# Performance work log

Hardware: AMD Instinct MI355X
Metric: run time of the kernel (lower is better)

Reference implementation:

```python
import jax, jax.numpy as jnp
import numpy as np
from jax import lax

NF, CF, LAT = 128, 3, 512          # n_filter, sobel c_factor (id+gx+gy), lat_size
NL, NC = 3, 4                      # n_layers (img 64 -> 3), n_calls
B, IMG, CH = 16, 64, 3
FIN, FH, FOUT = NF * CF, NF, 2 * NF  # dyna/res block in, hidden, out (gated -> 2*NF)
SPLIT = [NF, NF, NF, 1]
NOUT = sum(SPLIT)                  # 385
CS = NF + NF * 16 + NF * 16 + 16 * 16  # 4480 multi-cut state size
SEG = [FIN * FH, FH, FH * FH, FH, FH * FOUT, FOUT, FIN * FOUT, FOUT]
OFF = np.concatenate([[0], np.cumsum(SEG)]).astype(int)
K = int(OFF[-1])                   # hypernet output size (197376)

SOBEL_X = jnp.array([[-1., 0., 1.], [-2., 0., 2.], [-1., 0., 1.]], jnp.float32) / 8.0
SOBEL_Y = SOBEL_X.T
_g = np.exp(-0.5 * (np.arange(3) - 1.0) ** 2); _g /= _g.sum()
GAUSS = jnp.asarray(np.outer(_g, _g), jnp.float32)  # 3x3 gaussian, sigma=1


def dwconv(x, k2d):
    # depthwise conv, same 3x3 kernel for every channel, padding 1
    C = x.shape[1]
    k = jnp.broadcast_to(k2d.astype(x.dtype), (C, 1, 3, 3))
    return lax.conv_general_dilated(x, k, (1, 1), ((1, 1), (1, 1)),
                                    dimension_numbers=('NCHW', 'OIHW', 'NCHW'),
                                    feature_group_count=C)


def instnorm(x, eps=1e-5):
    m = x.mean((2, 3), keepdims=True)
    v = x.var((2, 3), keepdims=True)
    return (x - m) * lax.rsqrt(v + eps)


def conv1x1(x, w, b):  # w: [O, C]
    return jnp.einsum('bchw,oc->bohw', x, w) + b[None, :, None, None]


def lrb(x, w1, b1, w2, b2, wsc, bsc):  # LinearResidualBlock
    return x @ wsc.T + bsc + jax.nn.relu(x @ w1.T + b1) @ w2.T + b2


def _w(k, shape, fan_in):
    return jax.random.normal(k, shape, jnp.float32) / np.sqrt(fan_in)


def setup_inputs():
    ks = jax.random.split(jax.random.key(0), 24)
    z = lambda *s: jnp.zeros(s, jnp.float32)
    d = {}
    d['x'] = jax.random.normal(ks[0], (B, CH, IMG, IMG), jnp.float32)
    d['inj_lat'] = jax.random.normal(ks[1], (B, LAT), jnp.float32)
    d['leak_factor'] = jnp.float32(0.1)
    d['in_w'] = _w(ks[2], (NF, CH), CH); d['in_b'] = z(NF)
    d['fc_w1'] = _w(ks[3], (FH, FIN), FIN); d['fc_b1'] = z(FH)
    d['fc_w2'] = _w(ks[4], (FOUT, FH), FH); d['fc_b2'] = z(FOUT)
    d['fc_wsc'] = _w(ks[5], (FOUT, FIN), FIN); d['fc_bsc'] = z(FOUT)
    d['hyp_w'] = _w(ks[6], (K, LAT), LAT) * 0.1; d['hyp_b'] = z(K)
    d['lat_w'] = _w(ks[7], (NL * NC, LAT, LAT), LAT); d['lat_b'] = z(NL * NC, LAT)
    d['seed'] = _w(ks[8], (1, NF, 16, 16), NF)
    d['out_w'] = _w(ks[9], (NOUT, NF), NF); d['out_b'] = z(NOUT)
    d['l1_w1'] = _w(ks[10], (2 * LAT, CS), CS); d['l1_b1'] = z(2 * LAT)
    d['l1_w2'] = _w(ks[11], (LAT, 2 * LAT), 2 * LAT); d['l1_b2'] = z(LAT)
    d['l1_wsc'] = _w(ks[12], (LAT, CS), CS); d['l1_bsc'] = z(LAT)
    d['l2_w1'] = _w(ks[13], (LAT, LAT), LAT); d['l2_b1'] = z(LAT)
    d['l2_w2'] = _w(ks[14], (LAT, LAT), LAT); d['l2_b2'] = z(LAT)
    d['l2_wsc'] = _w(ks[15], (LAT, LAT), LAT); d['l2_bsc'] = z(LAT)
    d['fin_w'] = _w(ks[16], (LAT, LAT), LAT); d['fin_b'] = z(LAT)
    return d


def _forward(x, inj_lat, leak_factor, in_w, in_b, fc_w1, fc_b1, fc_w2, fc_b2,
             fc_wsc, fc_bsc, hyp_w, hyp_b, lat_w, lat_b, seed, out_w, out_b,
             l1_w1, l1_b1, l1_w2, l1_b2, l1_wsc, l1_bsc,
             l2_w1, l2_b1, l2_w2, l2_b2, l2_wsc, l2_bsc, fin_w, fin_b):
    out = conv1x1(x, in_w, in_b)
    leak = jnp.clip(leak_factor, 0.001, 1000.0)
    for c in range(NL * NC):
        # perception: identity + x/y sobel (c_factor=3), then instance norm
        p = jnp.concatenate([out, dwconv(out, SOBEL_X), dwconv(out, SOBEL_Y)], 1)
        p = instnorm(p)
        # static ResidualBlock (shared params)
        f = conv1x1(p, fc_wsc, fc_bsc) + conv1x1(jax.nn.relu(conv1x1(p, fc_w1, fc_b1)), fc_w2, fc_b2)
        # per-call latent expansion + hypernetwork -> per-sample 1x1 conv weights
        latc = inj_lat @ lat_w[c].T + lat_b[c]
        hk = latc @ hyp_w.T + hyp_b  # [B, K]
        w_in = hk[:, OFF[0]:OFF[1]].reshape(-1, FH, FIN); b_in = hk[:, OFF[1]:OFF[2]]
        w_md = hk[:, OFF[2]:OFF[3]].reshape(-1, FH, FH);  b_md = hk[:, OFF[3]:OFF[4]]
        w_ot = hk[:, OFF[4]:OFF[5]].reshape(-1, FOUT, FH); b_ot = hk[:, OFF[5]:OFF[6]]
        w_sc = hk[:, OFF[6]:OFF[7]].reshape(-1, FOUT, FIN); b_sc = hk[:, OFF[7]:OFF[8]]
        h = jax.nn.relu(jnp.einsum('bchw,boc->bohw', p, w_in) + b_in[:, :, None, None])
        h = jax.nn.relu(jnp.einsum('bchw,boc->bohw', h, w_md) + b_md[:, :, None, None])
        d = (jnp.einsum('bchw,boc->bohw', p, w_sc) + b_sc[:, :, None, None]
             + jnp.einsum('bchw,boc->bohw', h, w_ot) + b_ot[:, :, None, None])
        out_new = f + d  # [B, 2*NF, H, W]
        a, g = out_new[:, :NF], out_new[:, NF:]
        out = out + leak * (a * jax.nn.sigmoid(g))
        if c < NL * NC - 1 and c % NC == NC - 1:
            s = dwconv(out, GAUSS)
            # bilinear 0.5 downscale (align_corners=False) == 2x2 average
            Bn, C, H, W = s.shape
            out = s.reshape(Bn, C, H // 2, 2, W // 2, 2).mean((3, 5))
    out = out + seed  # broadcast seed [1, NF, 16, 16]
    o = conv1x1(out, out_w, out_b)  # [B, 385, 16, 16]
    f_, fh_, fw_, hw_ = o[:, :NF], o[:, NF:2 * NF], o[:, 2 * NF:3 * NF], o[:, 3 * NF:]
    bs = o.shape[0]
    cs = jnp.concatenate([f_.mean((2, 3)), fh_.mean(3).reshape(bs, -1),
                          fw_.mean(2).reshape(bs, -1), hw_.reshape(bs, -1)], 1)  # [B, 4480]
    hcs = lrb(cs, l1_w1, l1_b1, l1_w2, l1_b2, l1_wsc, l1_bsc)
    hcs = lrb(hcs, l2_w1, l2_b1, l2_w2, l2_b2, l2_wsc, l2_bsc)
    return hcs @ fin_w.T + fin_b  # [B, LAT]


def reference(x, inj_lat, leak_factor, in_w, in_b, fc_w1, fc_b1, fc_w2, fc_b2,
              fc_wsc, fc_bsc, hyp_w, hyp_b, lat_w, lat_b, seed, out_w, out_b,
              l1_w1, l1_b1, l1_w2, l1_b2, l1_wsc, l1_bsc,
              l2_w1, l2_b1, l2_w2, l2_b2, l2_wsc, l2_bsc, fin_w, fin_b):
    return _forward(x, inj_lat, leak_factor, in_w, in_b, fc_w1, fc_b1, fc_w2, fc_b2,
                    fc_wsc, fc_bsc, hyp_w, hyp_b, lat_w, lat_b, seed, out_w, out_b,
                    l1_w1, l1_b1, l1_w2, l1_b2, l1_wsc, l1_bsc,
                    l2_w1, l2_b1, l2_w2, l2_b2, l2_wsc, l2_bsc, fin_w, fin_b)
```

## Files before the change

### kernel.cpp

```cpp
#include <hip/hip_runtime.h>
#include <hip/hip_bf16.h>

typedef __hip_bfloat16 bf16;
typedef __attribute__((ext_vector_type(8))) short bf8_t;
typedef __attribute__((ext_vector_type(4))) float f4_t;

#define KHK 197376
#define OFF_WIN 0
#define OFF_BIN 49152
#define OFF_WMD 49280
#define OFF_BMD 65664
#define OFF_WOT 65792
#define OFF_BOT 98560
#define OFF_WSC 98816
#define OFF_BSC 197120

__device__ __forceinline__ float ldf(const float* p, size_t i){ return p[i]; }
__device__ __forceinline__ float ldf(const bf16* p, size_t i){ return __bfloat162float(p[i]); }
__device__ __forceinline__ void stf(float* p, size_t i, float v){ p[i] = v; }
__device__ __forceinline__ void stf(bf16* p, size_t i, float v){ p[i] = __float2bfloat16(v); }
__device__ __forceinline__ float b2f(short u){ return __uint_as_float(((unsigned)(unsigned short)u) << 16); }

typedef const __attribute__((address_space(1))) unsigned int* gas_t;
typedef __attribute__((address_space(3))) unsigned int* las_t;
__device__ __forceinline__ void gld_lds16(const void* g, void* l){
  __builtin_amdgcn_global_load_lds((gas_t)g, (las_t)l, 16, 0, 0);
}

struct Seg { const bf16* p; int klen; int ld; };

__global__ __launch_bounds__(256) void k_cvt_bf16(const float* __restrict__ in,
    bf16* __restrict__ out, size_t n){
  size_t stride = (size_t)gridDim.x * 256;
  for (size_t i = blockIdx.x*256ULL + threadIdx.x; i*8 < n; i += stride){
    float4 a = *reinterpret_cast<const float4*>(in + i*8);
    float4 c = *reinterpret_cast<const float4*>(in + i*8 + 4);
    union { bf8_t v; bf16 e[8]; } o;
    o.e[0]=__float2bfloat16(a.x); o.e[1]=__float2bfloat16(a.y);
    o.e[2]=__float2bfloat16(a.z); o.e[3]=__float2bfloat16(a.w);
    o.e[4]=__float2bfloat16(c.x); o.e[5]=__float2bfloat16(c.y);
    o.e[6]=__float2bfloat16(c.z); o.e[7]=__float2bfloat16(c.w);
    *reinterpret_cast<bf8_t*>(out + i*8) = o.v;
  }
}

__global__ __launch_bounds__(256) void k_in_conv(const float* __restrict__ x,
    const float* __restrict__ w, const float* __restrict__ b, float* __restrict__ out){
  int idx = blockIdx.x*256 + threadIdx.x;
  int c = idx & 127;
  int s = (idx >> 7) & 4095;
  int bi = idx >> 19;
  const float* xb = x + (size_t)bi*3*4096;
  out[idx] = b[c] + w[c*3]*xb[s] + w[c*3+1]*xb[4096+s] + w[c*3+2]*xb[8192+s];
}

__global__ __launch_bounds__(256) void k_sobel4(const float* __restrict__ src,
    bf16* __restrict__ p, int H, int S){
  int idx = blockIdx.x*256 + threadIdx.x;
  int c4 = (idx & 31) * 4;
  int s = (idx >> 5) % S;
  int b = idx / (S*32);
  int y = s / H, x = s - y*H;
  const float* sb = src + (size_t)b*S*128 + c4;
  float4 n[3][3];
  #pragma unroll
  for (int dy=0; dy<3; dy++)
    #pragma unroll
    for (int dx=0; dx<3; dx++){
      int yy = y + dy - 1, xx = x + dx - 1;
      if (yy>=0 && yy<H && xx>=0 && xx<H)
        n[dy][dx] = *reinterpret_cast<const float4*>(sb + (size_t)(yy*H+xx)*128);
      else
        n[dy][dx] = (float4){0.f,0.f,0.f,0.f};
    }
  float v0[4], sx[4], sy[4];
  #pragma unroll
  for (int q = 0; q < 4; q++){
    float e00=((const float*)&n[0][0])[q], e01=((const float*)&n[0][1])[q], e02=((const float*)&n[0][2])[q];
    float e10=((const float*)&n[1][0])[q], e11=((const float*)&n[1][1])[q], e12=((const float*)&n[1][2])[q];
    float e20=((const float*)&n[2][0])[q], e21=((const float*)&n[2][1])[q], e22=((const float*)&n[2][2])[q];
    v0[q] = e11;
    sx[q] = (-e00 + e02 - 2.f*e10 + 2.f*e12 - e20 + e22) * 0.125f;
    sy[q] = (-e00 - 2.f*e01 - e02 + e20 + 2.f*e21 + e22) * 0.125f;
  }
  bf16* pb = p + ((size_t)b*S + s)*384;
  union { unsigned long long u; bf16 e[4]; } o0, o1, o2;
  #pragma unroll
  for (int q = 0; q < 4; q++){
    o0.e[q] = __float2bfloat16(v0[q]);
    o1.e[q] = __float2bfloat16(sx[q]);
    o2.e[q] = __float2bfloat16(sy[q]);
  }
  *reinterpret_cast<unsigned long long*>(pb + c4)       = o0.u;
  *reinterpret_cast<unsigned long long*>(pb + 128 + c4) = o1.u;
  *reinterpret_cast<unsigned long long*>(pb + 256 + c4) = o2.u;
}

__global__ __launch_bounds__(256) void k_stats(const bf16* __restrict__ P_,
    float* __restrict__ SUMS, int S){
  __shared__ float sS[384], sQ[384];
  int b = blockIdx.y;
  int chunk = S >> 4;
  int s0 = blockIdx.x * chunk;
  int t = threadIdx.x;
  for (int i = t; i < 384; i += 256){ sS[i] = 0.f; sQ[i] = 0.f; }
  __syncthreads();
  if (t < 240){
    int oct = t % 48, ls = t / 48;
    int c8 = oct*8;
    float as[8] = {}, qs[8] = {};
    for (int s = s0 + ls; s < s0 + chunk; s += 5){
      bf8_t v = *reinterpret_cast<const bf8_t*>(P_ + ((size_t)b*S + s)*384 + c8);
      #pragma unroll
      for (int i=0;i<8;i++){ float f = b2f(v[i]); as[i]+=f; qs[i]+=f*f; }
    }
    #pragma unroll
    for (int i=0;i<8;i++){ atomicAdd(&sS[c8+i], as[i]); atomicAdd(&sQ[c8+i], qs[i]); }
  }
  __syncthreads();
  for (int i = t; i < 384; i += 256){
    atomicAdd(&SUMS[((size_t)b*384+i)*2],   sS[i]);
    atomicAdd(&SUMS[((size_t)b*384+i)*2+1], sQ[i]);
  }
}

__global__ __launch_bounds__(256) void k_hyper_all(const float* __restrict__ hw,
    const float* __restrict__ hb, const bf16* __restrict__ latb,
    bf16* __restrict__ hk_all){
  __shared__ float Sw[128][17];
  int h0 = blockIdx.x * 128;
  int tid = threadIdx.x, wid = tid >> 6, lane = tid & 63;
  int lr = lane & 15, lg = lane >> 4;
  f4_t acc[2][12];
  #pragma unroll
  for (int f=0; f<2; f++)
    #pragma unroll
    for (int j=0; j<12; j++) acc[f][j] = (f4_t){0.f,0.f,0.f,0.f};
  for (int k0 = 0; k0 < 512; k0 += 32){
    bf8_t af[2];
    #pragma unroll
    for (int f = 0; f < 2; f++){
      int h = h0 + wid*32 + f*16 + lr;
      const float* src = hw + (size_t)h*512 + k0 + lg*8;
      float4 x0 = *reinterpret_cast<const float4*>(src);
      float4 x1 = *reinterpret_cast<const float4*>(src + 4);
      union { bf8_t v; bf16 e[8]; } o;
      o.e[0]=__float2bfloat16(x0.x); o.e[1]=__float2bfloat16(x0.y);
      o.e[2]=__float2bfloat16(x0.z); o.e[3]=__float2bfloat16(x0.w);
      o.e[4]=__float2bfloat16(x1.x); o.e[5]=__float2bfloat16(x1.y);
      o.e[6]=__float2bfloat16(x1.z); o.e[7]=__float2bfloat16(x1.w);
      af[f] = o.v;
    }
    #pragma unroll
    for (int j = 0; j < 12; j++){
      bf8_t bv = *reinterpret_cast<const bf8_t*>(latb + (size_t)(j*16 + lr)*512 + k0 + lg*8);
      acc[0][j] = __builtin_amdgcn_mfma_f32_16x16x32_bf16(af[0], bv, acc[0][j], 0, 0, 0);
      acc[1][j] = __builtin_amdgcn_mfma_f32_16x16x32_bf16(af[1], bv, acc[1][j], 0, 0, 0);
    }
  }
  for (int j = 0; j < 12; j++){
    __syncthreads();
    #pragma unroll
    for (int f = 0; f < 2; f++)
      #pragma unroll
      for (int r = 0; r < 4; r++)
        Sw[wid*32 + f*16 + lg*4 + r][lr] = acc[f][j][r];
    __syncthreads();
    int bb = tid >> 4, h8 = (tid & 15) * 8;
    union { bf8_t v; bf16 e[8]; } o;
    #pragma unroll
    for (int i = 0; i < 8; i++)
      o.e[i] = __float2bfloat16(hb[h0 + h8 + i] + Sw[h8 + i][bb]);
    *reinterpret_cast<bf8_t*>(hk_all + ((size_t)j*16 + bb)*KHK + h0 + h8) = o.v;
  }
}

__global__ __launch_bounds__(256) void k_latall(const float* __restrict__ inj,
    const float* __restrict__ lat_w, const float* __restrict__ lat_b,
    bf16* __restrict__ LATB){
  int gwave = (int)((blockIdx.x*256 + threadIdx.x) >> 6);
  int lane = threadIdx.x & 63;
  int c = gwave >> 9, o = gwave & 511;
  const float* wr = lat_w + (size_t)c*262144 + (size_t)o*512;
  float acc[16] = {};
  for (int k = lane; k < 512; k += 64){
    float wv = wr[k];
    #pragma unroll
    for (int b = 0; b < 16; b++) acc[b] += wv * inj[b*512 + k];
  }
  #pragma unroll
  for (int b = 0; b < 16; b++)
    for (int off = 32; off > 0; off >>= 1) acc[b] += __shfl_down(acc[b], off);
  if (lane == 0){
    float bv = lat_b[c*512 + o];
    #pragma unroll
    for (int b = 0; b < 16; b++)
      LATB[(size_t)c*8192 + b*512 + o] = __float2bfloat16(acc[b] + bv);
  }
}

__global__ __launch_bounds__(256) void k_xform(
    const float* __restrict__ fc_w1, const float* __restrict__ fc_b1,
    const float* __restrict__ fc_w2, const float* __restrict__ fc_b2,
    const float* __restrict__ fc_wsc, const float* __restrict__ fc_bsc,
    const bf16* __restrict__ HK_, const float* __restrict__ SUMS, float Sf,
    bf16* __restrict__ Wstack, float* __restrict__ bstack,
    bf16* __restrict__ Wbig, float* __restrict__ bbig,
    bf16* __restrict__ Wmd, float* __restrict__ bmd){
  int gw = (blockIdx.x*256 + threadIdx.x) >> 6;
  int lane = threadIdx.x & 63;
  float invSf = 1.f / Sf;
  if (gw < 4096){
    int b = gw >> 8, o = gw & 255;
    const float* su = SUMS + (size_t)b*768;
    const bf16* hkb = HK_ + (size_t)b*KHK;
    float b0 = (o < 128) ? fc_b1[o] : ldf(hkb, OFF_BIN + (o-128));
    float accv = 0.f;
    bf16* dst = Wstack + ((size_t)b*256 + o)*384;
    for (int k = lane; k < 384; k += 64){
      float m = su[k*2] * invSf;
      float iv = rsqrtf(fmaxf(su[k*2+1]*invSf - m*m, 0.f) + 1e-5f);
      float wv = (o < 128) ? fc_w1[(size_t)o*384 + k]
                           : ldf(hkb, OFF_WIN + (size_t)(o-128)*384 + k);
      float w = wv * iv;
      accv += w * m;
      dst[k] = __float2bfloat16(w);
    }
    for (int off=32; off>0; off>>=1) accv += __shfl_down(accv, off);
    if (lane==0) bstack[b*256+o] = b0 - accv;
  } else if (gw < 8192){
    int r = gw - 4096; int b = r >> 8, o = r & 255;
    const float* su = SUMS + (size_t)b*768;
    const bf16* hkb = HK_ + (size_t)b*KHK;
    int cc = o & 127;
    int nr = ((cc >> 4) << 5) + ((o >> 7) << 4) + (cc & 15);
    bf16* dst = Wbig + ((size_t)b*256 + nr)*640;
    float accv = 0.f;
    for (int k = lane; k < 384; k += 64){
      float m = su[k*2] * invSf;
      float iv = rsqrtf(fmaxf(su[k*2+1]*invSf - m*m, 0.f) + 1e-5f);
      float w = (fc_wsc[(size_t)o*384 + k] + ldf(hkb, OFF_WSC + (size_t)o*384 + k)) * iv;
      accv += w * m;
      dst[k] = __float2bfloat16(w);
    }
    for (int k = lane; k < 128; k += 64){
      dst[384+k] = __float2bfloat16(fc_w2[(size_t)o*128 + k]);
      dst[512+k] = hkb[OFF_WOT + (size_t)o*128 + k];
    }
    for (int off=32; off>0; off>>=1) accv += __shfl_down(accv, off);
    if (lane==0) bbig[b*256+nr] = fc_bsc[o] + ldf(hkb, OFF_BSC+o) + fc_b2[o]
                                  + ldf(hkb, OFF_BOT+o) - accv;
  } else {
    int r = gw - 8192; int b = r >> 7, o = r & 127;
    const bf16* hkb = HK_ + (size_t)b*KHK;
    bf16* dst = Wmd + ((size_t)b*128 + o)*128;
    for (int k = lane; k < 128; k += 64)
      dst[k] = hkb[OFF_WMD + (size_t)o*128 + k];
    if (lane==0) bmd[b*128+o] = ldf(hkb, OFF_BMD + o);
  }
}

template<int RELU, int NSEG, class TOUT>
__global__ __launch_bounds__(256) void k_mfgemm(
    Seg s1, Seg s2, Seg s3,
    const bf16* __restrict__ W, long long wbstride, int Ktot,
    const float* __restrict__ bias, int bbstride,
    TOUT* __restrict__ OUTp, int ldc, int Mout, int S){
  __shared__ short As[128][32];
  __shared__ short Bs[128][32];
  int b  = blockIdx.z;
  int s0 = blockIdx.x * 128;
  int n0 = blockIdx.y * 128;
  int tid = threadIdx.x;
  int wid = tid >> 6, lane = tid & 63;
  int wrow = (wid >> 1) * 64;
  int wcol = (wid & 1) * 64;
  int lr = lane & 15, lg = lane >> 4;
  int r0 = wid*32 + (lane >> 2);
  int c8 = (lane & 3) * 8;
  const bf16* Wb = W + (size_t)b * wbstride;
  f4_t acc[4][4] = {{}};
  int kbase = 0;
  #pragma unroll
  for (int si = 0; si < NSEG; si++){
    Seg sg = (si == 0) ? s1 : (si == 1) ? s2 : s3;
    const bf16* INb = sg.p + (size_t)b * S * sg.ld;
    const bf16* gA0 = INb + (size_t)(s0 + r0) * sg.ld + c8;
    const bf16* gA1 = INb + (size_t)(s0 + r0 + 16) * sg.ld + c8;
    const bf16* gB0 = Wb + (size_t)(n0 + r0) * Ktot + kbase + c8;
    const bf16* gB1 = Wb + (size_t)(n0 + r0 + 16) * Ktot + kbase + c8;
    for (int k0 = 0; k0 < sg.klen; k0 += 32){
      gld_lds16(gA0 + k0, &As[wid*32][0]);
      gld_lds16(gA1 + k0, &As[wid*32 + 16][0]);
      gld_lds16(gB0 + k0, &Bs[wid*32][0]);
      gld_lds16(gB1 + k0, &Bs[wid*32 + 16][0]);
      __syncthreads();
      bf8_t af[4], bfv[4];
      #pragma unroll
      for (int i = 0; i < 4; i++) af[i]  = *(const bf8_t*)(&As[wrow + i*16 + lr][lg*8]);
      #pragma unroll
      for (int j = 0; j < 4; j++) bfv[j] = *(const bf8_t*)(&Bs[wcol + j*16 + lr][lg*8]);
      #pragma unroll
      for (int i = 0; i < 4; i++)
        #pragma unroll
        for (int j = 0; j < 4; j++)
          acc[i][j] = __builtin_amdgcn_mfma_f32_16x16x32_bf16(af[i], bfv[j], acc[i][j], 0, 0, 0);
      __syncthreads();
    }
    kbase += sg.klen;
  }
  #pragma unroll
  for (int j = 0; j < 4; j++){
    int n = n0 + wcol + j*16 + lr;
    if (n >= Mout) continue;
    float bv = bias[(size_t)b * bbstride + n];
    #pragma unroll
    for (int i = 0; i < 4; i++){
      int sr = s0 + wrow + i*16 + lg*4;
      size_t base = ((size_t)b * S + sr) * ldc + n;
      #pragma unroll
      for (int r = 0; r < 4; r++){
        float v = acc[i][j][r] + bv;
        if (RELU) v = fmaxf(v, 0.f);
        stf(OUTp, base + (size_t)r * ldc, v);
      }
    }
  }
}

__global__ __launch_bounds__(256) void k_mfgemm23(
    const bf16* __restrict__ P_, const bf16* __restrict__ HG_,
    const bf16* __restrict__ Wmd, const float* __restrict__ bmd,
    const bf16* __restrict__ Wbig, const float* __restrict__ bbig,
    float* __restrict__ OUTf, int S, const float* __restrict__ leakp){
  __shared__ short As[128][32];
  __shared__ short Bs[128][32];
  __shared__ short G2t[128][136];
  int b  = blockIdx.z;
  int s0 = blockIdx.x * 128;
  int n0 = blockIdx.y * 128;
  int tid = threadIdx.x;
  int wid = tid >> 6, lane = tid & 63;
  int wrow = (wid >> 1) * 64;
  int wcol = (wid & 1) * 64;
  int lr = lane & 15, lg = lane >> 4;
  int r0 = wid*32 + (lane >> 2);
  int c8 = (lane & 3) * 8;
  bf16* G2b = (bf16*)&G2t[0][0];
  f4_t acc[4][4] = {{}};
  {
    const bf16* gA0 = HG_ + ((size_t)b*S + s0 + r0) * 256 + 128 + c8;
    const bf16* gA1 = gA0 + (size_t)16 * 256;
    const bf16* gB0 = Wmd + (size_t)b*16384 + (size_t)r0 * 128 + c8;
    const bf16* gB1 = gB0 + 16*128;
    for (int k0 = 0; k0 < 128; k0 += 32){
      gld_lds16(gA0 + k0, &As[wid*32][0]);
      gld_lds16(gA1 + k0, &As[wid*32 + 16][0]);
      gld_lds16(gB0 + k0, &Bs[wid*32][0]);
      gld_lds16(gB1 + k0, &Bs[wid*32 + 16][0]);
      __syncthreads();
      bf8_t af[4], bfv[4];
      #pragma unroll
      for (int i = 0; i < 4; i++) af[i]  = *(const bf8_t*)(&As[wrow + i*16 + lr][lg*8]);
      #pragma unroll
      for (int j = 0; j < 4; j++) bfv[j] = *(const bf8_t*)(&Bs[wcol + j*16 + lr][lg*8]);
      #pragma unroll
      for (int i = 0; i < 4; i++)
        #pragma unroll
        for (int j = 0; j < 4; j++)
          acc[i][j] = __builtin_amdgcn_mfma_f32_16x16x32_bf16(af[i], bfv[j], acc[i][j], 0, 0, 0);
      __syncthreads();
    }
    const float* bmdb = bmd + b*128;
    #pragma unroll
    for (int j = 0; j < 4; j++){
      int col = wcol + j*16 + lr;
      float bv = bmdb[col];
      #pragma unroll
      for (int i = 0; i < 4; i++){
        int row = wrow + i*16 + lg*4;
        #pragma unroll
        for (int r = 0; r < 4; r++)
          stf(G2b, (size_t)(row + r)*136 + col, fmaxf(acc[i][j][r] + bv, 0.f));
      }
    }
    #pragma unroll
    for (int i = 0; i < 4; i++)
      #pragma unroll
      for (int j = 0; j < 4; j++)
        acc[i][j] = (f4_t){0.f,0.f,0.f,0.f};
    __syncthreads();
  }
  const bf16* Wb = Wbig + (size_t)b * 163840;
  {
    const bf16* gA0 = P_ + ((size_t)b*S + s0 + r0) * 384 + c8;
    const bf16* gA1 = gA0 + (size_t)16 * 384;
    const bf16* gB0 = Wb + (size_t)(n0 + r0) * 640 + c8;
    const bf16* gB1 = gB0 + (size_t)16*640;
    for (int k0 = 0; k0 < 384; k0 += 32){
      gld_lds16(gA0 + k0, &As[wid*32][0]);
      gld_lds16(gA1 + k0, &As[wid*32 + 16][0]);
      gld_lds16(gB0 + k0, &Bs[wid*32][0]);
      gld_lds16(gB1 + k0, &Bs[wid*32 + 16][0]);
      __syncthreads();
      bf8_t af[4], bfv[4];
      #pragma unroll
      for (int i = 0; i < 4; i++) af[i]  = *(const bf8_t*)(&As[wrow + i*16 + lr][lg*8]);
      #pragma unroll
      for (int j = 0; j < 4; j++) bfv[j] = *(const bf8_t*)(&Bs[wcol + j*16 + lr][lg*8]);
      #pragma unroll
      for (int i = 0; i < 4; i++)
        #pragma unroll
        for (int j = 0; j < 4; j++)
          acc[i][j] = __builtin_amdgcn_mfma_f32_16x16x32_bf16(af[i], bfv[j], acc[i][j], 0, 0, 0);
      __syncthreads();
    }
  }
  {
    const bf16* gA0 = HG_ + ((size_t)b*S + s0 + r0) * 256 + c8;
    const bf16* gA1 = gA0 + (size_t)16 * 256;
    const bf16* gB0 = Wb + (size_t)(n0 + r0) * 640 + 384 + c8;
    const bf16* gB1 = gB0 + (size_t)16*640;
    for (int k0 = 0; k0 < 128; k0 += 32){
      gld_lds16(gA0 + k0, &As[wid*32][0]);
      gld_lds16(gA1 + k0, &As[wid*32 + 16][0]);
      gld_lds16(gB0 + k0, &Bs[wid*32][0]);
      gld_lds16(gB1 + k0, &Bs[wid*32 + 16][0]);
      __syncthreads();
      bf8_t af[4], bfv[4];
      #pragma unroll
      for (int i = 0; i < 4; i++) af[i]  = *(const bf8_t*)(&As[wrow + i*16 + lr][lg*8]);
      #pragma unroll
      for (int j = 0; j < 4; j++) bfv[j] = *(const bf8_t*)(&Bs[wcol + j*16 + lr][lg*8]);
      #pragma unroll
      for (int i = 0; i < 4; i++)
        #pragma unroll
        for (int j = 0; j < 4; j++)
          acc[i][j] = __builtin_amdgcn_mfma_f32_16x16x32_bf16(af[i], bfv[j], acc[i][j], 0, 0, 0);
      __syncthreads();
    }
  }
  {
    const bf16* gB0 = Wb + (size_t)(n0 + r0) * 640 + 512 + c8;
    const bf16* gB1 = gB0 + (size_t)16*640;
    for (int k0 = 0; k0 < 128; k0 += 32){
      gld_lds16(gB0 + k0, &Bs[wid*32][0]);
      gld_lds16(gB1 + k0, &Bs[wid*32 + 16][0]);
      __syncthreads();
      bf8_t af[4], bfv[4];
      #pragma unroll
      for (int i = 0; i < 4; i++) af[i]  = *(const bf8_t*)(&G2t[wrow + i*16 + lr][k0 + lg*8]);
      #pragma unroll
      for (int j = 0; j < 4; j++) bfv[j] = *(const bf8_t*)(&Bs[wcol + j*16 + lr][lg*8]);
      #pragma unroll
      for (int i = 0; i < 4; i++)
        #pragma unroll
        for (int j = 0; j < 4; j++)
          acc[i][j] = __builtin_amdgcn_mfma_f32_16x16x32_bf16(af[i], bfv[j], acc[i][j], 0, 0, 0);
      __syncthreads();
    }
  }
  float leak = fminf(fmaxf(leakp[0], 0.001f), 1000.f);
  #pragma unroll
  for (int jp = 0; jp < 2; jp++){
    int na = n0 + wcol + jp*32 + lr;
    float bva = bbig[(size_t)b * 256 + na];
    float bvg = bbig[(size_t)b * 256 + na + 16];
    int chan = ((n0 + wcol) >> 1) + jp*16 + lr;
    #pragma unroll
    for (int i = 0; i < 4; i++){
      int sr = s0 + wrow + i*16 + lg*4;
      #pragma unroll
      for (int r = 0; r < 4; r++){
        float av = acc[i][jp*2][r]   + bva;
        float gv = acc[i][jp*2+1][r] + bvg;
        size_t oidx = ((size_t)b * S + sr + r) * 128 + chan;
        OUTf[oidx] += leak * av * (1.f / (1.f + expf(-gv)));
      }
    }
  }
}

__global__ __launch_bounds__(256) void k_blurpool(const float* __restrict__ src,
    float* __restrict__ dst, int H2, int S2){
  const float g[3] = {0.27406862f, 0.45186276f, 0.27406862f};
  int idx = blockIdx.x*256 + threadIdx.x;
  int c = idx & 127;
  int s2 = (idx >> 7) % S2;
  int b = idx / (S2*128);
  int y2 = s2 / H2, x2 = s2 - y2*H2;
  int H = H2*2;
  const float* sb = src + (size_t)b*(H*H)*128 + c;
  float acc = 0.f;
  #pragma unroll
  for (int dy2 = 0; dy2 < 2; dy2++)
    #pragma unroll
    for (int dx2 = 0; dx2 < 2; dx2++){
      int y = 2*y2 + dy2, x = 2*x2 + dx2;
      float bl = 0.f;
      #pragma unroll
      for (int i = 0; i < 3; i++)
        #pragma unroll
        for (int j = 0; j < 3; j++){
          int yy = y + i - 1, xx = x + j - 1;
          float v = (yy>=0 && yy<H && xx>=0 && xx<H) ? sb[(size_t)(yy*H+xx)*128] : 0.f;
          bl += v * g[i] * g[j];
        }
      acc += bl;
    }
  dst[idx] = acc * 0.25f;
}

__global__ __launch_bounds__(256) void k_seedcvt(const float* __restrict__ in,
    const float* __restrict__ seed, bf16* __restrict__ out){
  int idx = blockIdx.x*256 + threadIdx.x;
  int c = idx & 127;
  int s = (idx >> 7) & 255;
  out[idx] = __float2bfloat16(in[idx] + seed[c*256 + s]);
}

__global__ __launch_bounds__(256) void k_build_cs(const float* __restrict__ O,
    float* __restrict__ cs){
  int b = blockIdx.x;
  const float* Ob = O + (size_t)b*256*385;
  for (int id = threadIdx.x; id < 4480; id += 256){
    float v;
    if (id < 128){
      float s = 0; for (int t = 0; t < 256; t++) s += Ob[(size_t)t*385 + id];
      v = s * (1.f/256.f);
    } else if (id < 2176){
      int r = id - 128; int c = r >> 4, h = r & 15;
      float s = 0; for (int w = 0; w < 16; w++) s += Ob[(size_t)(h*16+w)*385 + 128 + c];
      v = s * (1.f/16.f);
    } else if (id < 4224){
      int r = id - 2176; int c = r >> 4, w = r & 15;
      float s = 0; for (int h = 0; h < 16; h++) s += Ob[(size_t)(h*16+w)*385 + 256 + c];
      v = s * (1.f/16.f);
    } else {
      v = Ob[(size_t)(id - 4224)*385 + 384];
    }
    cs[b*4480 + id] = v;
  }
}

template<int RELU, int ACCUM, class TOUT>
__global__ __launch_bounds__(256) void k_rowgemm(const float* __restrict__ IN,
    const float* __restrict__ W,
    const float* __restrict__ bias,
    TOUT* __restrict__ OUT, int M, int K){
  int wave = (int)((blockIdx.x*256 + threadIdx.x) >> 6);
  int lane = threadIdx.x & 63;
  if (wave >= M) return;
  const float* wr = W + (size_t)wave*K;
  float acc[16] = {};
  for (int k = lane; k < K; k += 64){
    float wv = wr[k];
    #pragma unroll
    for (int b = 0; b < 16; b++) acc[b] += wv * IN[b*K + k];
  }
  #pragma unroll
  for (int b = 0; b < 16; b++)
    for (int off = 32; off > 0; off >>= 1) acc[b] += __shfl_down(acc[b], off);
  if (lane == 0){
    float bv = bias[wave];
    #pragma unroll
    for (int b = 0; b < 16; b++){
      float v = acc[b] + bv;
      if (RELU) v = fmaxf(v, 0.f);
      size_t oi = (size_t)b*M + wave;
      if (ACCUM) v += ldf(OUT, oi);
      stf(OUT, oi, v);
    }
  }
}

template<int RELU1>
__global__ __launch_bounds__(256) void k_rowgemm2(const float* __restrict__ IN,
    const float* __restrict__ W1, const float* __restrict__ b1, float* __restrict__ O1, int M1,
    const float* __restrict__ W2, const float* __restrict__ b2, float* __restrict__ O2, int M2,
    int K){
  int wave = (int)((blockIdx.x*256 + threadIdx.x) >> 6);
  int lane = threadIdx.x & 63;
  if (wave >= M1 + M2) return;
  int second = (wave >= M1);
  int o = second ? (wave - M1) : wave;
  const float* wr = (second ? W2 : W1) + (size_t)o*K;
  float acc[16] = {};
  for (int k = lane; k < K; k += 64){
    float wv = wr[k];
    #pragma unroll
    for (int b = 0; b < 16; b++) acc[b] += wv * IN[b*K + k];
  }
  #pragma unroll
  for (int b = 0; b < 16; b++)
    for (int off = 32; off > 0; off >>= 1) acc[b] += __shfl_down(acc[b], off);
  if (lane == 0){
    float bv = second ? b2[o] : b1[o];
    float* OUT = second ? O2 : O1;
    int M = second ? M2 : M1;
    #pragma unroll
    for (int b = 0; b < 16; b++){
      float v = acc[b] + bv;
      if (RELU1 && !second) v = fmaxf(v, 0.f);
      OUT[(size_t)b*M + o] = v;
    }
  }
}

extern "C" void kernel_launch(void* const* d_in, const int* in_sizes, int n_in,
                              void* d_out, int out_size, void* d_ws, size_t ws_size,
                              hipStream_t stream){
  (void)in_sizes; (void)n_in; (void)out_size; (void)ws_size;
  const float* x      = (const float*)d_in[0];
  const float* inj    = (const float*)d_in[1];
  const float* leakp  = (const float*)d_in[2];
  const float* in_w   = (const float*)d_in[3];
  const float* in_b   = (const float*)d_in[4];
  const float* fc_w1  = (const float*)d_in[5];
  const float* fc_b1  = (const float*)d_in[6];
  const float* fc_w2  = (const float*)d_in[7];
  const float* fc_b2  = (const float*)d_in[8];
  const float* fc_wsc = (const float*)d_in[9];
  const float* fc_bsc = (const float*)d_in[10];
  const float* hyp_w  = (const float*)d_in[11];
  const float* hyp_b  = (const float*)d_in[12];
  const float* lat_w  = (const float*)d_in[13];
  const float* lat_b  = (const float*)d_in[14];
  const float* seed   = (const float*)d_in[15];
  const float* out_w  = (const float*)d_in[16];
  const float* out_b  = (const float*)d_in[17];
  const float* l1_w1  = (const float*)d_in[18];
  const float* l1_b1  = (const float*)d_in[19];
  const float* l1_w2  = (const float*)d_in[20];
  const float* l1_b2  = (const float*)d_in[21];
  const float* l1_wsc = (const float*)d_in[22];
  const float* l1_bsc = (const float*)d_in[23];
  const float* l2_w1  = (const float*)d_in[24];
  const float* l2_b1  = (const float*)d_in[25];
  const float* l2_w2  = (const float*)d_in[26];
  const float* l2_b2  = (const float*)d_in[27];
  const float* l2_wsc = (const float*)d_in[28];
  const float* l2_bsc = (const float*)d_in[29];
  const float* fin_w  = (const float*)d_in[30];
  const float* fin_b  = (const float*)d_in[31];

  char* ws = (char*)d_ws;
  float* OUT    = (float*)(ws);
  bf16*  P      = (bf16*)(ws + 33554432UL);
  bf16*  HG     = (bf16*)(ws + 83886080UL);
  bf16*  HKALL  = (bf16*)(ws + 134217728UL);
  bf16*  WSTK   = (bf16*)(ws + 285802496UL);
  bf16*  WBIG   = (bf16*)(ws + 288948224UL);
  bf16*  WMD    = (bf16*)(ws + 294191104UL);
  float* BSTK   = (float*)(ws + 294715392UL);
  float* BBIG   = (float*)(ws + 294731776UL);
  float* BMD    = (float*)(ws + 294748160UL);
  bf16*  LATB   = (bf16*)(ws + 294805504UL);
  bf16*  OUTB   = (bf16*)(ws + 295002112UL);
  float* OHEAD  = (float*)(ws + 296050688UL);
  bf16*  OWB    = (bf16*)(ws + 302358528UL);
  float* CS     = (float*)(ws + 302457088UL);
  float* T1     = (float*)(ws + 302743808UL);
  float* HCS    = (float*)(ws + 302809344UL);
  float* HCS2   = (float*)(ws + 302842112UL);
  float* SUMS12 = (float*)(ws + 302874880UL);
  float* OUT2   = (float*)(ws + 310378496UL);

  k_cvt_bf16<<<32, 256, 0, stream>>>(out_w, OWB, 49280ULL);
  k_in_conv<<<32768, 256, 0, stream>>>(x, in_w, in_b, OUT);

  k_latall<<<1536, 256, 0, stream>>>(inj, lat_w, lat_b, LATB);
  k_hyper_all<<<1542, 256, 0, stream>>>(hyp_w, hyp_b, LATB, HKALL);
  (void)hipMemsetAsync(SUMS12, 0, 12*16*384*2*sizeof(float), stream);

  float* cur = OUT;
  float* alt = OUT2;
  int H = 64;
  for (int c = 0; c < 12; c++){
    int S = H*H;
    float* SUMS = SUMS12 + (size_t)c*16*768;
    k_sobel4<<<(16*S*32)/256, 256, 0, stream>>>(cur, P, H, S);
    k_stats<<<dim3(16,16), 256, 0, stream>>>(P, SUMS, S);
    k_xform<<<2560, 256, 0, stream>>>(fc_w1, fc_b1, fc_w2, fc_b2, fc_wsc, fc_bsc,
                                      HKALL + (size_t)c*16*KHK, SUMS, (float)S,
                                      WSTK, BSTK, WBIG, BBIG, WMD, BMD);
    Seg segP  = {P, 384, 384};
    k_mfgemm<1,1,bf16><<<dim3(S/128, 2, 16), 256, 0, stream>>>(
        segP, segP, segP, WSTK, 98304LL, 384, BSTK, 256, HG, 256, 256, S);
    k_mfgemm23<<<dim3(S/128, 2, 16), 256, 0, stream>>>(
        P, HG, WMD, BMD, WBIG, BBIG, cur, S, leakp);
    if (c == 3 || c == 7){
      int H2 = H/2, S2 = S/4;
      k_blurpool<<<(16*S2*128)/256, 256, 0, stream>>>(cur, alt, H2, S2);
      float* t = cur; cur = alt; alt = t;
      H = H2;
    }
  }

  k_seedcvt<<<2048, 256, 0, stream>>>(cur, seed, OUTB);
  Seg segO = {OUTB, 128, 128};
  k_mfgemm<0,1,float><<<dim3(2, 4, 16), 256, 0, stream>>>(
      segO, segO, segO, OWB, 0LL, 128, out_b, 0, OHEAD, 385, 385, 256);
  k_build_cs<<<16, 256, 0, stream>>>(OHEAD, CS);

  k_rowgemm2<1><<<384, 256, 0, stream>>>(CS, l1_w1, l1_b1, T1, 1024,
                                         l1_wsc, l1_bsc, HCS, 512, 4480);
  k_rowgemm<0,1,float><<<128, 256, 0, stream>>>(T1, l1_w2, l1_b2, HCS, 512, 1024);
  k_rowgemm2<1><<<256, 256, 0, stream>>>(HCS, l2_w1, l2_b1, T1, 512,
                                         l2_wsc, l2_bsc, HCS2, 512, 512);
  k_rowgemm<0,1,float><<<128, 256, 0, stream>>>(T1, l2_w2, l2_b2, HCS2, 512, 512);
  k_rowgemm<0,0,float><<<128, 256, 0, stream>>>(HCS2, fin_w, fin_b, (float*)d_out, 512, 512);
}
```

Baseline: 1.482 ms.

## Widen per-layer GEMM tiles to cover all 256 output columns per block

The two per-call GEMM kernels now launch 512-thread blocks that each cover a 128-row by 256-column output tile, instead of two 256-thread blocks that split the columns. The A tiles (P and HG activations) are now loaded once per row tile rather than twice. In the fused kernel the 128x128 middle-layer GEMM and its ReLU no longer run redundantly in both column blocks. In exchange there are half as many blocks, more LDS per block and larger workgroups, which may reduce occupancy and latency hiding. The multi-segment template path is also simplified to a single segment.

```diff
diff --git a/kernel.cpp b/kernel.cpp
--- a/kernel.cpp
+++ b/kernel.cpp
@@ -260,10 +260,193 @@
   }
 }
 
-template<int RELU, int NSEG, class TOUT>
+__global__ __launch_bounds__(512) void k_gemm1(const bf16* __restrict__ P_,
+    const bf16* __restrict__ W, const float* __restrict__ bias,
+    bf16* __restrict__ HGo, int S){
+  __shared__ short As[128][32];
+  __shared__ short Bs[256][32];
+  int b = blockIdx.z, s0 = blockIdx.x * 128;
+  int tid = threadIdx.x, wid = tid >> 6, lane = tid & 63;
+  int wrow = (wid >> 2) * 64, wcol = (wid & 3) * 64;
+  int lr = lane & 15, lg = lane >> 4;
+  int r0 = tid >> 2, c8 = (tid & 3) * 8;
+  const bf16* Wb = W + (size_t)b * 98304;
+  f4_t acc[4][4] = {{}};
+  const bf16* gA  = P_ + ((size_t)b*S + s0 + r0) * 384 + c8;
+  const bf16* gB0 = Wb + (size_t)r0 * 384 + c8;
+  const bf16* gB1 = Wb + (size_t)(128 + r0) * 384 + c8;
+  for (int k0 = 0; k0 < 384; k0 += 32){
+    gld_lds16(gA + k0,  &As[wid*16][0]);
+    gld_lds16(gB0 + k0, &Bs[wid*16][0]);
+    gld_lds16(gB1 + k0, &Bs[128 + wid*16][0]);
+    __syncthreads();
+    bf8_t af[4], bfv[4];
+    #pragma unroll
+    for (int i = 0; i < 4; i++) af[i]  = *(const bf8_t*)(&As[wrow + i*16 + lr][lg*8]);
+    #pragma unroll
+    for (int j = 0; j < 4; j++) bfv[j] = *(const bf8_t*)(&Bs[wcol + j*16 + lr][lg*8]);
+    #pragma unroll
+    for (int i = 0; i < 4; i++)
+      #pragma unroll
+      for (int j = 0; j < 4; j++)
+        acc[i][j] = __builtin_amdgcn_mfma_f32_16x16x32_bf16(af[i], bfv[j], acc[i][j], 0, 0, 0);
+    __syncthreads();
+  }
+  #pragma unroll
+  for (int j = 0; j < 4; j++){
+    int n = wcol + j*16 + lr;
+    float bv = bias[(size_t)b * 256 + n];
+    #pragma unroll
+    for (int i = 0; i < 4; i++){
+      int sr = s0 + wrow + i*16 + lg*4;
+      size_t base = ((size_t)b * S + sr) * 256 + n;
+      #pragma unroll
+      for (int r = 0; r < 4; r++)
+        stf(HGo, base + (size_t)r * 256, fmaxf(acc[i][j][r] + bv, 0.f));
+    }
+  }
+}
+
+__global__ __launch_bounds__(512) void k_gemm23(
+    const bf16* __restrict__ P_, const bf16* __restrict__ HG_,
+    const bf16* __restrict__ Wmd, const float* __restrict__ bmd,
+    const bf16* __restrict__ Wbig, const float* __restrict__ bbig,
+    float* __restrict__ OUTf, int S, const float* __restrict__ leakp){
+  __shared__ short As[128][32];
+  __shared__ short Bs[256][32];
+  __shared__ short G2t[128][136];
+  int b = blockIdx.z, s0 = blockIdx.x * 128;
+  int tid = threadIdx.x, wid = tid >> 6, lane = tid & 63;
+  int lr = lane & 15, lg = lane >> 4;
+  int r0 = tid >> 2, c8 = (tid & 3) * 8;
+  bf16* G2b = (bf16*)&G2t[0][0];
+  {
+    int wrowA = (wid >> 1) * 32, wcolA = (wid & 1) * 64;
+    f4_t accA[2][4] = {{}};
+    const bf16* gA = HG_ + ((size_t)b*S + s0 + r0) * 256 + 128 + c8;
+    const bf16* gB = Wmd + (size_t)b*16384 + (size_t)r0 * 128 + c8;
+    for (int k0 = 0; k0 < 128; k0 += 32){
+      gld_lds16(gA + k0, &As[wid*16][0]);
+      gld_lds16(gB + k0, &Bs[wid*16][0]);
+      __syncthreads();
+      bf8_t af[2], bfv[4];
+      #pragma unroll
+      for (int i = 0; i < 2; i++) af[i]  = *(const bf8_t*)(&As[wrowA + i*16 + lr][lg*8]);
+      #pragma unroll
+      for (int j = 0; j < 4; j++) bfv[j] = *(const bf8_t*)(&Bs[wcolA + j*16 + lr][lg*8]);
+      #pragma unroll
+      for (int i = 0; i < 2; i++)
+        #pragma unroll
+        for (int j = 0; j < 4; j++)
+          accA[i][j] = __builtin_amdgcn_mfma_f32_16x16x32_bf16(af[i], bfv[j], accA[i][j], 0, 0, 0);
+      __syncthreads();
+    }
+    const float* bmdb = bmd + b*128;
+    #pragma unroll
+    for (int j = 0; j < 4; j++){
+      int col = wcolA + j*16 + lr;
+      float bv = bmdb[col];
+      #pragma unroll
+      for (int i = 0; i < 2; i++){
+        int row = wrowA + i*16 + lg*4;
+        #pragma unroll
+        for (int r = 0; r < 4; r++)
+          stf(G2b, (size_t)(row + r)*136 + col, fmaxf(accA[i][j][r] + bv, 0.f));
+      }
+    }
+    __syncthreads();
+  }
+  int wrow = (wid >> 2) * 64, wcol = (wid & 3) * 64;
+  f4_t acc[4][4] = {{}};
+  const bf16* Wb = Wbig + (size_t)b * 163840;
+  {
+    const bf16* gA  = P_ + ((size_t)b*S + s0 + r0) * 384 + c8;
+    const bf16* gB0 = Wb + (size_t)r0 * 640 + c8;
+    const bf16* gB1 = Wb + (size_t)(128 + r0) * 640 + c8;
+    for (int k0 = 0; k0 < 384; k0 += 32){
+      gld_lds16(gA + k0,  &As[wid*16][0]);
+      gld_lds16(gB0 + k0, &Bs[wid*16][0]);
+      gld_lds16(gB1 + k0, &Bs[128 + wid*16][0]);
+      __syncthreads();
+      bf8_t af[4], bfv[4];
+      #pragma unroll
+      for (int i = 0; i < 4; i++) af[i]  = *(const bf8_t*)(&As[wrow + i*16 + lr][lg*8]);
+      #pragma unroll
+      for (int j = 0; j < 4; j++) bfv[j] = *(const bf8_t*)(&Bs[wcol + j*16 + lr][lg*8]);
+      #pragma unroll
+      for (int i = 0; i < 4; i++)
+        #pragma unroll
+        for (int j = 0; j < 4; j++)
+          acc[i][j] = __builtin_amdgcn_mfma_f32_16x16x32_bf16(af[i], bfv[j], acc[i][j], 0, 0, 0);
+      __syncthreads();
+    }
+  }
+  {
+    const bf16* gA  = HG_ + ((size_t)b*S + s0 + r0) * 256 + c8;
+    const bf16* gB0 = Wb + (size_t)r0 * 640 + 384 + c8;
+    const bf16* gB1 = Wb + (size_t)(128 + r0) * 640 + 384 + c8;
+    for (int k0 = 0; k0 < 128; k0 += 32){
+      gld_lds16(gA + k0,  &As[wid*16][0]);
+      gld_lds16(gB0 + k0, &Bs[wid*16][0]);
+      gld_lds16(gB1 + k0, &Bs[128 + wid*16][0]);
+      __syncthreads();
+      bf8_t af[4], bfv[4];
+      #pragma unroll
+      for (int i = 0; i < 4; i++) af[i]  = *(const bf8_t*)(&As[wrow + i*16 + lr][lg*8]);
+      #pragma unroll
+      for (int j = 0; j < 4; j++) bfv[j] = *(const bf8_t*)(&Bs[wcol + j*16 + lr][lg*8]);
+      #pragma unroll
+      for (int i = 0; i < 4; i++)
+        #pragma unroll
+        for (int j = 0; j < 4; j++)
+          acc[i][j] = __builtin_amdgcn_mfma_f32_16x16x32_bf16(af[i], bfv[j], acc[i][j], 0, 0, 0);
+      __syncthreads();
+    }
+  }
+  {
+    const bf16* gB0 = Wb + (size_t)r0 * 640 + 512 + c8;
+    const bf16* gB1 = Wb + (size_t)(128 + r0) * 640 + 512 + c8;
+    for (int k0 = 0; k0 < 128; k0 += 32){
+      gld_lds16(gB0 + k0, &Bs[wid*16][0]);
+      gld_lds16(gB1 + k0, &Bs[128 + wid*16][0]);
+      __syncthreads();
+      bf8_t af[4], bfv[4];
+      #pragma unroll
+      for (int i = 0; i < 4; i++) af[i]  = *(const bf8_t*)(&G2t[wrow + i*16 + lr][k0 + lg*8]);
+      #pragma unroll
+      for (int j = 0; j < 4; j++) bfv[j] = *(const bf8_t*)(&Bs[wcol + j*16 + lr][lg*8]);
+      #pragma unroll
+      for (int i = 0; i < 4; i++)
+        #pragma unroll
+        for (int j = 0; j < 4; j++)
+          acc[i][j] = __builtin_amdgcn_mfma_f32_16x16x32_bf16(af[i], bfv[j], acc[i][j], 0, 0, 0);
+      __syncthreads();
+    }
+  }
+  float leak = fminf(fmaxf(leakp[0], 0.001f), 1000.f);
+  #pragma unroll
+  for (int jp = 0; jp < 2; jp++){
+    int na = wcol + jp*32 + lr;
+    float bva = bbig[(size_t)b * 256 + na];
+    float bvg = bbig[(size_t)b * 256 + na + 16];
+    int chan = (wcol >> 1) + jp*16 + lr;
+    #pragma unroll
+    for (int i = 0; i < 4; i++){
+      int sr = s0 + wrow + i*16 + lg*4;
+      #pragma unroll
+      for (int r = 0; r < 4; r++){
+        float av = acc[i][jp*2][r]   + bva;
+        float gv = acc[i][jp*2+1][r] + bvg;
+        size_t oidx = ((size_t)b * S + sr + r) * 128 + chan;
+        OUTf[oidx] += leak * av * (1.f / (1.f + expf(-gv)));
+      }
+    }
+  }
+}
+
+template<int RELU, class TOUT>
 __global__ __launch_bounds__(256) void k_mfgemm(
-    Seg s1, Seg s2, Seg s3,
-    const bf16* __restrict__ W, long long wbstride, int Ktot,
+    Seg s1, const bf16* __restrict__ W, long long wbstride, int Ktot,
     const float* __restrict__ bias, int bbstride,
     TOUT* __restrict__ OUTp, int ldc, int Mout, int S){
   __shared__ short As[128][32];
@@ -280,34 +463,28 @@
   int c8 = (lane & 3) * 8;
   const bf16* Wb = W + (size_t)b * wbstride;
   f4_t acc[4][4] = {{}};
-  int kbase = 0;
-  #pragma unroll
-  for (int si = 0; si < NSEG; si++){
-    Seg sg = (si == 0) ? s1 : (si == 1) ? s2 : s3;
-    const bf16* INb = sg.p + (size_t)b * S * sg.ld;
-    const bf16* gA0 = INb + (size_t)(s0 + r0) * sg.ld + c8;
-    const bf16* gA1 = INb + (size_t)(s0 + r0 + 16) * sg.ld + c8;
-    const bf16* gB0 = Wb + (size_t)(n0 + r0) * Ktot + kbase + c8;
-    const bf16* gB1 = Wb + (size_t)(n0 + r0 + 16) * Ktot + kbase + c8;
-    for (int k0 = 0; k0 < sg.klen; k0 += 32){
-      gld_lds16(gA0 + k0, &As[wid*32][0]);
-      gld_lds16(gA1 + k0, &As[wid*32 + 16][0]);
-      gld_lds16(gB0 + k0, &Bs[wid*32][0]);
-      gld_lds16(gB1 + k0, &Bs[wid*32 + 16][0]);
-      __syncthreads();
-      bf8_t af[4], bfv[4];
-      #pragma unroll
-      for (int i = 0; i < 4; i++) af[i]  = *(const bf8_t*)(&As[wrow + i*16 + lr][lg*8]);
-      #pragma unroll
-      for (int j = 0; j < 4; j++) bfv[j] = *(const bf8_t*)(&Bs[wcol + j*16 + lr][lg*8]);
-      #pragma unroll
-      for (int i = 0; i < 4; i++)
-        #pragma unroll
-        for (int j = 0; j < 4; j++)
-          acc[i][j] = __builtin_amdgcn_mfma_f32_16x16x32_bf16(af[i], bfv[j], acc[i][j], 0, 0, 0);
-      __syncthreads();
-    }
-    kbase += sg.klen;
+  const bf16* INb = s1.p + (size_t)b * S * s1.ld;
+  const bf16* gA0 = INb + (size_t)(s0 + r0) * s1.ld + c8;
+  const bf16* gA1 = INb + (size_t)(s0 + r0 + 16) * s1.ld + c8;
+  const bf16* gB0 = Wb + (size_t)(n0 + r0) * Ktot + c8;
+  const bf16* gB1 = Wb + (size_t)(n0 + r0 + 16) * Ktot + c8;
+  for (int k0 = 0; k0 < s1.klen; k0 += 32){
+    gld_lds16(gA0 + k0, &As[wid*32][0]);
+    gld_lds16(gA1 + k0, &As[wid*32 + 16][0]);
+    gld_lds16(gB0 + k0, &Bs[wid*32][0]);
+    gld_lds16(gB1 + k0, &Bs[wid*32 + 16][0]);
+    __syncthreads();
+    bf8_t af[4], bfv[4];
+    #pragma unroll
+    for (int i = 0; i < 4; i++) af[i]  = *(const bf8_t*)(&As[wrow + i*16 + lr][lg*8]);
+    #pragma unroll
+    for (int j = 0; j < 4; j++) bfv[j] = *(const bf8_t*)(&Bs[wcol + j*16 + lr][lg*8]);
+    #pragma unroll
+    for (int i = 0; i < 4; i++)
+      #pragma unroll
+      for (int j = 0; j < 4; j++)
+        acc[i][j] = __builtin_amdgcn_mfma_f32_16x16x32_bf16(af[i], bfv[j], acc[i][j], 0, 0, 0);
+    __syncthreads();
   }
   #pragma unroll
   for (int j = 0; j < 4; j++){
@@ -323,159 +500,6 @@
         float v = acc[i][j][r] + bv;
         if (RELU) v = fmaxf(v, 0.f);
         stf(OUTp, base + (size_t)r * ldc, v);
-      }
-    }
-  }
-}
-
-__global__ __launch_bounds__(256) void k_mfgemm23(
-    const bf16* __restrict__ P_, const bf16* __restrict__ HG_,
-    const bf16* __restrict__ Wmd, const float* __restrict__ bmd,
-    const bf16* __restrict__ Wbig, const float* __restrict__ bbig,
-    float* __restrict__ OUTf, int S, const float* __restrict__ leakp){
-  __shared__ short As[128][32];
-  __shared__ short Bs[128][32];
-  __shared__ short G2t[128][136];
-  int b  = blockIdx.z;
-  int s0 = blockIdx.x * 128;
-  int n0 = blockIdx.y * 128;
-  int tid = threadIdx.x;
-  int wid = tid >> 6, lane = tid & 63;
-  int wrow = (wid >> 1) * 64;
-  int wcol = (wid & 1) * 64;
-  int lr = lane & 15, lg = lane >> 4;
-  int r0 = wid*32 + (lane >> 2);
-  int c8 = (lane & 3) * 8;
-  bf16* G2b = (bf16*)&G2t[0][0];
-  f4_t acc[4][4] = {{}};
-  {
-    const bf16* gA0 = HG_ + ((size_t)b*S + s0 + r0) * 256 + 128 + c8;
-    const bf16* gA1 = gA0 + (size_t)16 * 256;
-    const bf16* gB0 = Wmd + (size_t)b*16384 + (size_t)r0 * 128 + c8;
-    const bf16* gB1 = gB0 + 16*128;
-    for (int k0 = 0; k0 < 128; k0 += 32){
-      gld_lds16(gA0 + k0, &As[wid*32][0]);
-      gld_lds16(gA1 + k0, &As[wid*32 + 16][0]);
-      gld_lds16(gB0 + k0, &Bs[wid*32][0]);
-      gld_lds16(gB1 + k0, &Bs[wid*32 + 16][0]);
-      __syncthreads();
-      bf8_t af[4], bfv[4];
-      #pragma unroll
-      for (int i = 0; i < 4; i++) af[i]  = *(const bf8_t*)(&As[wrow + i*16 + lr][lg*8]);
-      #pragma unroll
-      for (int j = 0; j < 4; j++) bfv[j] = *(const bf8_t*)(&Bs[wcol + j*16 + lr][lg*8]);
-      #pragma unroll
-      for (int i = 0; i < 4; i++)
-        #pragma unroll
-        for (int j = 0; j < 4; j++)
-          acc[i][j] = __builtin_amdgcn_mfma_f32_16x16x32_bf16(af[i], bfv[j], acc[i][j], 0, 0, 0);
-      __syncthreads();
-    }
-    const float* bmdb = bmd + b*128;
-    #pragma unroll
-    for (int j = 0; j < 4; j++){
-      int col = wcol + j*16 + lr;
-      float bv = bmdb[col];
-      #pragma unroll
-      for (int i = 0; i < 4; i++){
-        int row = wrow + i*16 + lg*4;
-        #pragma unroll
-        for (int r = 0; r < 4; r++)
-          stf(G2b, (size_t)(row + r)*136 + col, fmaxf(acc[i][j][r] + bv, 0.f));
-      }
-    }
-    #pragma unroll
-    for (int i = 0; i < 4; i++)
-      #pragma unroll
-      for (int j = 0; j < 4; j++)
-        acc[i][j] = (f4_t){0.f,0.f,0.f,0.f};
-    __syncthreads();
-  }
-  const bf16* Wb = Wbig + (size_t)b * 163840;
-  {
-    const bf16* gA0 = P_ + ((size_t)b*S + s0 + r0) * 384 + c8;
-    const bf16* gA1 = gA0 + (size_t)16 * 384;
-    const bf16* gB0 = Wb + (size_t)(n0 + r0) * 640 + c8;
-    const bf16* gB1 = gB0 + (size_t)16*640;
-    for (int k0 = 0; k0 < 384; k0 += 32){
-      gld_lds16(gA0 + k0, &As[wid*32][0]);
-      gld_lds16(gA1 + k0, &As[wid*32 + 16][0]);
-      gld_lds16(gB0 + k0, &Bs[wid*32][0]);
-      gld_lds16(gB1 + k0, &Bs[wid*32 + 16][0]);
-      __syncthreads();
-      bf8_t af[4], bfv[4];
-      #pragma unroll
-      for (int i = 0; i < 4; i++) af[i]  = *(const bf8_t*)(&As[wrow + i*16 + lr][lg*8]);
-      #pragma unroll
-      for (int j = 0; j < 4; j++) bfv[j] = *(const bf8_t*)(&Bs[wcol + j*16 + lr][lg*8]);
-      #pragma unroll
-      for (int i = 0; i < 4; i++)
-        #pragma unroll
-        for (int j = 0; j < 4; j++)
-          acc[i][j] = __builtin_amdgcn_mfma_f32_16x16x32_bf16(af[i], bfv[j], acc[i][j], 0, 0, 0);
-      __syncthreads();
-    }
-  }
-  {
-    const bf16* gA0 = HG_ + ((size_t)b*S + s0 + r0) * 256 + c8;
-    const bf16* gA1 = gA0 + (size_t)16 * 256;
-    const bf16* gB0 = Wb + (size_t)(n0 + r0) * 640 + 384 + c8;
-    const bf16* gB1 = gB0 + (size_t)16*640;
-    for (int k0 = 0; k0 < 128; k0 += 32){
-      gld_lds16(gA0 + k0, &As[wid*32][0]);
-      gld_lds16(gA1 + k0, &As[wid*32 + 16][0]);
-      gld_lds16(gB0 + k0, &Bs[wid*32][0]);
-      gld_lds16(gB1 + k0, &Bs[wid*32 + 16][0]);
-      __syncthreads();
-      bf8_t af[4], bfv[4];
-      #pragma unroll
-      for (int i = 0; i < 4; i++) af[i]  = *(const bf8_t*)(&As[wrow + i*16 + lr][lg*8]);
-      #pragma unroll
-      for (int j = 0; j < 4; j++) bfv[j] = *(const bf8_t*)(&Bs[wcol + j*16 + lr][lg*8]);
-      #pragma unroll
-      for (int i = 0; i < 4; i++)
-        #pragma unroll
-        for (int j = 0; j < 4; j++)
-          acc[i][j] = __builtin_amdgcn_mfma_f32_16x16x32_bf16(af[i], bfv[j], acc[i][j], 0, 0, 0);
-      __syncthreads();
-    }
-  }
-  {
-    const bf16* gB0 = Wb + (size_t)(n0 + r0) * 640 + 512 + c8;
-    const bf16* gB1 = gB0 + (size_t)16*640;
-    for (int k0 = 0; k0 < 128; k0 += 32){
-      gld_lds16(gB0 + k0, &Bs[wid*32][0]);
-      gld_lds16(gB1 + k0, &Bs[wid*32 + 16][0]);
-      __syncthreads();
-      bf8_t af[4], bfv[4];
-      #pragma unroll
-      for (int i = 0; i < 4; i++) af[i]  = *(const bf8_t*)(&G2t[wrow + i*16 + lr][k0 + lg*8]);
-      #pragma unroll
-      for (int j = 0; j < 4; j++) bfv[j] = *(const bf8_t*)(&Bs[wcol + j*16 + lr][lg*8]);
-      #pragma unroll
-      for (int i = 0; i < 4; i++)
-        #pragma unroll
-        for (int j = 0; j < 4; j++)
-          acc[i][j] = __builtin_amdgcn_mfma_f32_16x16x32_bf16(af[i], bfv[j], acc[i][j], 0, 0, 0);
-      __syncthreads();
-    }
-  }
-  float leak = fminf(fmaxf(leakp[0], 0.001f), 1000.f);
-  #pragma unroll
-  for (int jp = 0; jp < 2; jp++){
-    int na = n0 + wcol + jp*32 + lr;
-    float bva = bbig[(size_t)b * 256 + na];
-    float bvg = bbig[(size_t)b * 256 + na + 16];
-    int chan = ((n0 + wcol) >> 1) + jp*16 + lr;
-    #pragma unroll
-    for (int i = 0; i < 4; i++){
-      int sr = s0 + wrow + i*16 + lg*4;
-      #pragma unroll
-      for (int r = 0; r < 4; r++){
-        float av = acc[i][jp*2][r]   + bva;
-        float gv = acc[i][jp*2+1][r] + bvg;
-        size_t oidx = ((size_t)b * S + sr + r) * 128 + chan;
-        OUTf[oidx] += leak * av * (1.f / (1.f + expf(-gv)));
       }
     }
   }
@@ -684,10 +708,8 @@
     k_xform<<<2560, 256, 0, stream>>>(fc_w1, fc_b1, fc_w2, fc_b2, fc_wsc, fc_bsc,
                                       HKALL + (size_t)c*16*KHK, SUMS, (float)S,
                                       WSTK, BSTK, WBIG, BBIG, WMD, BMD);
-    Seg segP  = {P, 384, 384};
-    k_mfgemm<1,1,bf16><<<dim3(S/128, 2, 16), 256, 0, stream>>>(
-        segP, segP, segP, WSTK, 98304LL, 384, BSTK, 256, HG, 256, 256, S);
-    k_mfgemm23<<<dim3(S/128, 2, 16), 256, 0, stream>>>(
+    k_gemm1<<<dim3(S/128, 1, 16), 512, 0, stream>>>(P, WSTK, BSTK, HG, S);
+    k_gemm23<<<dim3(S/128, 1, 16), 512, 0, stream>>>(
         P, HG, WMD, BMD, WBIG, BBIG, cur, S, leakp);
     if (c == 3 || c == 7){
       int H2 = H/2, S2 = S/4;
@@ -699,8 +721,8 @@
 
   k_seedcvt<<<2048, 256, 0, stream>>>(cur, seed, OUTB);
   Seg segO = {OUTB, 128, 128};
-  k_mfgemm<0,1,float><<<dim3(2, 4, 16), 256, 0, stream>>>(
-      segO, segO, segO, OWB, 0LL, 128, out_b, 0, OHEAD, 385, 385, 256);
+  k_mfgemm<0,float><<<dim3(2, 4, 16), 256, 0, stream>>>(
+      segO, OWB, 0LL, 128, out_b, 0, OHEAD, 385, 385, 256);
   k_build_cs<<<16, 256, 0, stream>>>(OHEAD, CS);
 
   k_rowgemm2<1><<<384, 256, 0, stream>>>(CS, l1_w1, l1_b1, T1, 1024,
```

Measured after the change: 1.500 ms. No clear change (+1.2%).
